# Optimization experiments

Measured on AMD Instinct MI355X. Metric: run time of the kernel, lower is better.

Reference implementation:

```python
import jax, jax.numpy as jnp
import numpy as np

N_NODES = 50000
N_EDGES = 800000
N_GRAPHS = 256
IN_DIM = 128
HID = 128
BN_EPS = 1e-5


def setup_inputs() -> dict:
    key = jax.random.key(0)
    ks = jax.random.split(key, 12)
    s = 1.0 / np.sqrt(HID)
    feats = jax.random.normal(ks[0], (N_NODES, IN_DIM), jnp.float32)
    src = jax.random.randint(ks[1], (2, N_EDGES), 0, N_NODES)
    dst = jax.random.randint(ks[2], (2, N_EDGES), 0, N_NODES)
    graph_ids = jnp.sort(jax.random.randint(ks[3], (N_NODES,), 0, N_GRAPHS))
    eps = jnp.full((2, 2), 0.1, jnp.float32)
    Wa = jax.random.normal(ks[4], (2, 2, IN_DIM, HID), jnp.float32) * s
    ba = jnp.zeros((2, 2, HID), jnp.float32)
    bng = jnp.ones((2, 2, HID), jnp.float32)
    bnb = jnp.zeros((2, 2, HID), jnp.float32)
    Wb = jax.random.normal(ks[5], (2, 2, HID, HID), jnp.float32) * s
    bb = jnp.zeros((2, 2, HID), jnp.float32)
    oW1 = jax.random.normal(ks[6], (2 * HID, HID), jnp.float32) * (1.0 / np.sqrt(2 * HID))
    ob1 = jnp.zeros((HID,), jnp.float32)
    oW2 = jax.random.normal(ks[7], (HID, HID), jnp.float32) * s
    ob2 = jnp.zeros((HID,), jnp.float32)
    oW3 = jax.random.normal(ks[8], (HID, 1), jnp.float32) * s
    ob3 = jnp.zeros((1,), jnp.float32)
    return {"feats": feats, "src": src, "dst": dst, "graph_ids": graph_ids,
            "n_graphs": N_GRAPHS, "eps": eps, "Wa": Wa, "ba": ba, "bng": bng,
            "bnb": bnb, "Wb": Wb, "bb": bb, "oW1": oW1, "ob1": ob1,
            "oW2": oW2, "ob2": ob2, "oW3": oW3, "ob3": ob3}


def _gin_layer(h, s, d, eps_l, Wa_l, ba_l, g_l, be_l, Wb_l, bb_l, relu_out):
    # sum-aggregate messages from src to dst over edge list
    N = h.shape[0]
    agg = jax.ops.segment_sum(h[s], d, num_segments=N)  # [N, D]
    x = (1.0 + eps_l) * h + agg
    # MLP_Layer: Linear -> BatchNorm(training stats) -> ReLU -> Linear
    x = x @ Wa_l + ba_l
    mu = jnp.mean(x, axis=0)
    var = jnp.var(x, axis=0)
    x = (x - mu) * jax.lax.rsqrt(var + BN_EPS) * g_l + be_l
    x = jax.nn.relu(x)
    x = x @ Wb_l + bb_l
    return jax.nn.relu(x) if relu_out else x  # GINConv activation (gin1 only)


def reference(feats, src, dst, graph_ids, n_graphs, eps, Wa, ba, bng, bnb,
              Wb, bb, oW1, ob1, oW2, ob2, oW3, ob3):
    outs = []
    for e in range(2):  # one BTGINs encoder per bottom edge type
        h = feats
        for l in range(2):  # gin1 (ReLU) then gin2 (no activation)
            h = _gin_layer(h, src[e], dst[e], eps[e, l], Wa[e, l], ba[e, l],
                           bng[e, l], bnb[e, l], Wb[e, l], bb[e, l], relu_out=(l == 0))
        outs.append(h)
    h = jnp.concatenate(outs, axis=-1)  # [N, 2*HID]
    # readout_nodes op='sum': per-graph segment sum
    hg = jax.ops.segment_sum(h, graph_ids, num_segments=n_graphs)  # [G, 2*HID]
    # out_layers: 3-layer MLP, no BN
    x = jax.nn.relu(hg @ oW1 + ob1)
    x = jax.nn.relu(x @ oW2 + ob2)
    return x @ oW3 + ob3  # [G, 1]
```

## Files before the change

kernel.cpp:

```cpp
#include <hip/hip_runtime.h>

#define NT 50000
#define NE 800000
#define NG 256
#define DIM 128
#define GEMM_B ((NT + 127) / 128)

#define NB 128
#define BW 391
#define PB 196
#define PCH 4096
#define HCN (NB * PB)

typedef short s16x8 __attribute__((ext_vector_type(8)));
typedef float f32x16 __attribute__((ext_vector_type(16)));

__device__ __forceinline__ unsigned short f32_to_bf16(float f) {
    unsigned int u = __float_as_uint(f);
    u += 0x7FFFu + ((u >> 16) & 1u);
    return (unsigned short)(u >> 16);
}
__device__ __forceinline__ float bf16_to_f32(unsigned short h) {
    return __uint_as_float(((unsigned int)h) << 16);
}

__global__ __launch_bounds__(256) void tobf16_kernel(const float* __restrict__ in,
                                                     unsigned short* __restrict__ out) {
    int i = blockIdx.x * 256 + threadIdx.x;
    if (i >= NT * 32) return;
    float4 v = ((const float4*)in)[i];
    ushort4 o;
    o.x = f32_to_bf16(v.x); o.y = f32_to_bf16(v.y);
    o.z = f32_to_bf16(v.z); o.w = f32_to_bf16(v.w);
    ((ushort4*)out)[i] = o;
}

__global__ __launch_bounds__(256) void csr_part_hist_kernel(
        const int* __restrict__ dstAll, int* __restrict__ hcoarseAll) {
    const int* dst = dstAll + (size_t)blockIdx.y * NE;
    int* hcoarse = hcoarseAll + (size_t)blockIdx.y * HCN;
    __shared__ int h[NB];
    if (threadIdx.x < NB) h[threadIdx.x] = 0;
    __syncthreads();
#pragma unroll
    for (int i = 0; i < PCH / 256; ++i) {
        int e = blockIdx.x * PCH + i * 256 + threadIdx.x;
        if (e < NE) atomicAdd(&h[dst[e] / BW], 1);
    }
    __syncthreads();
    if (threadIdx.x < NB)
        hcoarse[threadIdx.x * PB + blockIdx.x] = h[threadIdx.x];
}

__global__ __launch_bounds__(1024) void csr_scan_kernel(
        const int* __restrict__ hcoarseAll, int* __restrict__ offAll,
        int* __restrict__ bucketBaseAll, int* __restrict__ indptrAll) {
    const int* hcoarse = hcoarseAll + (size_t)blockIdx.x * HCN;
    int* off = offAll + (size_t)blockIdx.x * HCN;
    int* bucketBase = bucketBaseAll + (size_t)blockIdx.x * (NB + 1);
    int* indptr = indptrAll + (size_t)blockIdx.x * (NT + 1);
    __shared__ int ps[1024];
    int t = threadIdx.x;
    const int CH = (HCN + 1023) / 1024;
    int beg = t * CH, end = beg + CH; if (end > HCN) end = HCN;
    int s = 0;
    for (int i = beg; i < end; ++i) s += hcoarse[i];
    ps[t] = s;
    __syncthreads();
    for (int o = 1; o < 1024; o <<= 1) {
        int v = (t >= o) ? ps[t - o] : 0;
        __syncthreads();
        ps[t] += v;
        __syncthreads();
    }
    int run = (t == 0) ? 0 : ps[t - 1];
    for (int i = beg; i < end; ++i) {
        off[i] = run;
        if (i % PB == 0) bucketBase[i / PB] = run;
        run += hcoarse[i];
    }
    if (t == 1023) bucketBase[NB] = NE;
    if (t == 0) indptr[NT] = NE;
}

__global__ __launch_bounds__(256) void csr_scatter_kernel(
        const int* __restrict__ srcAll, const int* __restrict__ dstAll,
        const int* __restrict__ offAll, unsigned int* __restrict__ partAll) {
    const int* src = srcAll + (size_t)blockIdx.y * NE;
    const int* dst = dstAll + (size_t)blockIdx.y * NE;
    const int* off = offAll + (size_t)blockIdx.y * HCN;
    unsigned int* part = partAll + (size_t)blockIdx.y * NE;
    __shared__ int cur[NB];
    if (threadIdx.x < NB) cur[threadIdx.x] = off[threadIdx.x * PB + blockIdx.x];
    __syncthreads();
#pragma unroll
    for (int i = 0; i < PCH / 256; ++i) {
        int e = blockIdx.x * PCH + i * 256 + threadIdx.x;
        if (e < NE) {
            int d = dst[e];
            int b = d / BW;
            int pos = atomicAdd(&cur[b], 1);
            part[pos] = ((unsigned int)(d - b * BW) << 16) | (unsigned int)src[e];
        }
    }
}

__global__ __launch_bounds__(256) void csr_finalize_kernel(
        const unsigned int* __restrict__ partAll,
        const int* __restrict__ bucketBaseAll,
        int* __restrict__ indptrAll, int* __restrict__ esrcAll) {
    const unsigned int* part = partAll + (size_t)blockIdx.y * NE;
    const int* bucketBase = bucketBaseAll + (size_t)blockIdx.y * (NB + 1);
    int* indptr = indptrAll + (size_t)blockIdx.y * (NT + 1);
    int* esrc = esrcAll + (size_t)blockIdx.y * NE;
    __shared__ int cnt[512];
    __shared__ int excl[512];
    __shared__ int ps[256];
    __shared__ int cur[BW + 1];
    int b = blockIdx.x, t = threadIdx.x;
    int base = bucketBase[b];
    int n = bucketBase[b + 1] - base;
    cnt[t] = 0; cnt[t + 256] = 0;
    for (int j = t; j <= BW; j += 256) cur[j] = 0;
    __syncthreads();
    for (int i = t; i < n; i += 256) atomicAdd(&cnt[part[base + i] >> 16], 1);
    __syncthreads();
    int a0 = cnt[2 * t], a1 = cnt[2 * t + 1];
    ps[t] = a0 + a1;
    __syncthreads();
    for (int o = 1; o < 256; o <<= 1) {
        int v = (t >= o) ? ps[t - o] : 0;
        __syncthreads();
        ps[t] += v;
        __syncthreads();
    }
    int before = (t == 0) ? 0 : ps[t - 1];
    excl[2 * t] = before;
    excl[2 * t + 1] = before + a0;
    __syncthreads();
    int node0 = b * BW;
    for (int j = t; j < BW; j += 256) {
        int gn = node0 + j;
        if (gn < NT) indptr[gn] = base + excl[j];
    }
    for (int i = t; i < n; i += 256) {
        unsigned int pk = part[base + i];
        int dl = pk >> 16;
        int pos = atomicAdd(&cur[dl], 1);
        esrc[base + excl[dl] + pos] = (int)(pk & 0xFFFFu);
    }
}

__global__ __launch_bounds__(256) void agg_split_kernel(
        const float* __restrict__ h, long hStride,
        const unsigned short* __restrict__ hb, long hbStride,
        const int* __restrict__ indptr2, const int* __restrict__ esrc2,
        const float* __restrict__ eps_p, int l,
        unsigned short* __restrict__ xout2) {
    int e = blockIdx.y;
    const float* hs = h + (size_t)e * hStride;
    const unsigned short* hbs = hb + (size_t)e * hbStride;
    const int* indptr = indptr2 + (size_t)e * (NT + 1);
    const int* esrc = esrc2 + (size_t)e * NE;
    unsigned short* xo = xout2 + (size_t)e * NT * 256;
    int node = blockIdx.x * 4 + (threadIdx.x >> 6);
    if (node >= NT) return;
    int lane = threadIdx.x & 63;
    int half = lane >> 5, c = lane & 31;
    float s0 = 0.f, s1 = 0.f, s2 = 0.f, s3 = 0.f;
    if (half == 0) {
        float e1 = 1.0f + eps_p[e * 2 + l];
        float4 a = ((const float4*)hs)[(size_t)node * 32 + c];
        s0 = e1 * a.x; s1 = e1 * a.y; s2 = e1 * a.z; s3 = e1 * a.w;
    }
    int beg = indptr[node], end = indptr[node + 1];
    int deg = end - beg;
    int endFull = beg + (deg & ~15);
    int j = beg;
    for (; j < endFull; j += 16) {
        int b0 = j + half * 8;
        int idx[8];
#pragma unroll
        for (int k = 0; k < 8; ++k) idx[k] = esrc[b0 + k];
        ushort4 v[8];
#pragma unroll
        for (int k = 0; k < 8; ++k)
            v[k] = *(const ushort4*)(hbs + (size_t)idx[k] * 128 + c * 4);
#pragma unroll
        for (int k = 0; k < 8; ++k) {
            s0 += bf16_to_f32(v[k].x);
            s1 += bf16_to_f32(v[k].y);
            s2 += bf16_to_f32(v[k].z);
            s3 += bf16_to_f32(v[k].w);
        }
    }
    if (j < end) {
        int b0 = j + half * 8;
        int idx[8];
        float m[8];
#pragma unroll
        for (int k = 0; k < 8; ++k) {
            int jj = b0 + k;
            int ok = jj < end;
            idx[k] = esrc[ok ? jj : end - 1];
            m[k] = ok ? 1.f : 0.f;
        }
        ushort4 v[8];
#pragma unroll
        for (int k = 0; k < 8; ++k)
            v[k] = *(const ushort4*)(hbs + (size_t)idx[k] * 128 + c * 4);
#pragma unroll
        for (int k = 0; k < 8; ++k) {
            s0 = fmaf(bf16_to_f32(v[k].x), m[k], s0);
            s1 = fmaf(bf16_to_f32(v[k].y), m[k], s1);
            s2 = fmaf(bf16_to_f32(v[k].z), m[k], s2);
            s3 = fmaf(bf16_to_f32(v[k].w), m[k], s3);
        }
    }
    s0 += __shfl_xor(s0, 32);
    s1 += __shfl_xor(s1, 32);
    s2 += __shfl_xor(s2, 32);
    s3 += __shfl_xor(s3, 32);
    if (half == 0) {
        ushort4 hv, lv;
        hv.x = f32_to_bf16(s0); lv.x = f32_to_bf16(s0 - bf16_to_f32(hv.x));
        hv.y = f32_to_bf16(s1); lv.y = f32_to_bf16(s1 - bf16_to_f32(hv.y));
        hv.z = f32_to_bf16(s2); lv.z = f32_to_bf16(s2 - bf16_to_f32(hv.z));
        hv.w = f32_to_bf16(s3); lv.w = f32_to_bf16(s3 - bf16_to_f32(hv.w));
        *(ushort4*)(xo + (size_t)node * 256 + c * 4) = hv;
        *(ushort4*)(xo + (size_t)node * 256 + 128 + c * 4) = lv;
    }
}

__global__ __launch_bounds__(256) void bsplit_kernel(const float* __restrict__ Wa,
                                                     const float* __restrict__ Wb,
                                                     unsigned short* __restrict__ Bfrag,
                                                     const int* __restrict__ gid,
                                                     int* __restrict__ goff,
                                                     float* __restrict__ gsumAll) {
    if (blockIdx.x == 0) {
        int g = threadIdx.x;
        int lo = 0, hi = NT;
        while (lo < hi) {
            int mid = (lo + hi) >> 1;
            if (gid[mid] < g) lo = mid + 1; else hi = mid;
        }
        goff[g] = lo;
        if (g == 0) goff[NG] = NT;
    }
    if (blockIdx.x == 1) {
#pragma unroll
        for (int i = 0; i < 4; ++i) gsumAll[i * 256 + threadIdx.x] = 0.f;
    }
    int slot = blockIdx.x >> 3;
    int sub = blockIdx.x & 7;
    const float* W = (slot < 4) ? (Wa + (size_t)slot * DIM * DIM)
                                : (Wb + (size_t)(slot - 4) * DIM * DIM);
    unsigned short* out = Bfrag + (size_t)slot * 32768;
    for (int i = 0; i < 16; ++i) {
        int e = sub * 4096 + i * 256 + threadIdx.x;
        int kphys = e >> 7, n = e & 127;
        int k = kphys & 127;
        float wv = W[k * 128 + n];
        unsigned short hi = f32_to_bf16(wv);
        unsigned short val = (kphys < 128) ? hi : f32_to_bf16(wv - bf16_to_f32(hi));
        int nt = n >> 5, nin = n & 31;
        int kcp = kphys >> 4, kgp = (kphys >> 3) & 1, jj = kphys & 7;
        out[(size_t)(((nt * 16 + kcp) * 64) + kgp * 32 + nin) * 8 + jj] = val;
    }
}

template <int ASPLIT, int STATS, int RELU, int EMITB>
__global__ __launch_bounds__(256) void fused_gemm_kernel(
        const void* __restrict__ Asrc, long aStride,
        const unsigned short* __restrict__ BfragBase, int bOff, int l,
        const float* __restrict__ biasBase,
        const float* __restrict__ gsumBase,
        const float* __restrict__ gammaBase, const float* __restrict__ betaBase,
        float* __restrict__ C, long cStride,
        unsigned short* __restrict__ CBout, long cbStride,
        float* __restrict__ gsumOutBase) {
    __shared__ char smem[65536 + 1024];
    unsigned short* sB = (unsigned short*)smem;
    float* sBNa = (float*)(smem + 65536);
    float* sBNb = sBNa + 128;
    const int ety = blockIdx.y, wi = ety * 2 + l;
    const unsigned short* Bfrag = BfragBase + (size_t)(bOff + wi) * 32768;
    const float* bias = biasBase + (size_t)wi * DIM;
    const int tid = threadIdx.x;
    const int w = tid >> 6, lane = tid & 63;
    const int nin = lane & 31, kg = lane >> 5;
    const int row0 = blockIdx.x * 128;
    const int myrow = row0 + w * 32 + nin;
    const int rowc = myrow < NT ? myrow : NT - 1;

    {
        const uint4* Bg = (const uint4*)Bfrag;
        uint4* sB4 = (uint4*)smem;
#pragma unroll
        for (int i = 0; i < 16; ++i) sB4[tid + 256 * i] = Bg[tid + 256 * i];
    }

    s16x8 ahi[8], alo[8];
    if (ASPLIT) {
        const unsigned short* ar = (const unsigned short*)Asrc
                + (size_t)ety * aStride + (size_t)rowc * 256 + kg * 8;
#pragma unroll
        for (int kc = 0; kc < 8; ++kc) {
            ahi[kc] = *(const s16x8*)(ar + kc * 16);
            alo[kc] = *(const s16x8*)(ar + 128 + kc * 16);
        }
        __syncthreads();
    } else {
        const float* gsumIn = gsumBase + (size_t)wi * 256;
        if (tid < 128) {
            float mu = gsumIn[tid] * (1.0f / NT);
            float var = gsumIn[128 + tid] * (1.0f / NT) - mu * mu;
            float inv = rsqrtf(var + 1e-5f);
            float a = gammaBase[wi * DIM + tid] * inv;
            sBNa[tid] = a;
            sBNb[tid] = betaBase[wi * DIM + tid] - mu * a;
        }
        __syncthreads();
        const float* yr = (const float*)Asrc + (size_t)ety * aStride
                + (size_t)rowc * 128 + kg * 8;
#pragma unroll
        for (int kc = 0; kc < 8; ++kc) {
            int c0 = kc * 16 + kg * 8;
            float4 y0 = *(const float4*)(yr + kc * 16);
            float4 y1 = *(const float4*)(yr + kc * 16 + 4);
            float4 a0 = *(const float4*)(sBNa + c0);
            float4 a1 = *(const float4*)(sBNa + c0 + 4);
            float4 b0 = *(const float4*)(sBNb + c0);
            float4 b1 = *(const float4*)(sBNb + c0 + 4);
            float t[8];
            t[0] = fmaxf(0.f, fmaf(y0.x, a0.x, b0.x));
            t[1] = fmaxf(0.f, fmaf(y0.y, a0.y, b0.y));
            t[2] = fmaxf(0.f, fmaf(y0.z, a0.z, b0.z));
            t[3] = fmaxf(0.f, fmaf(y0.w, a0.w, b0.w));
            t[4] = fmaxf(0.f, fmaf(y1.x, a1.x, b1.x));
            t[5] = fmaxf(0.f, fmaf(y1.y, a1.y, b1.y));
            t[6] = fmaxf(0.f, fmaf(y1.z, a1.z, b1.z));
            t[7] = fmaxf(0.f, fmaf(y1.w, a1.w, b1.w));
            union { s16x8 v; unsigned short u[8]; } H, L;
#pragma unroll
            for (int q = 0; q < 8; ++q) {
                H.u[q] = f32_to_bf16(t[q]);
                L.u[q] = f32_to_bf16(t[q] - bf16_to_f32(H.u[q]));
            }
            ahi[kc] = H.v; alo[kc] = L.v;
        }
    }

    f32x16 acc[4];
#pragma unroll
    for (int nt = 0; nt < 4; ++nt)
#pragma unroll
        for (int r = 0; r < 16; ++r) acc[nt][r] = 0.f;

#pragma unroll
    for (int nt = 0; nt < 4; ++nt) {
        const unsigned short* bp = sB + (size_t)(nt * 16) * 512 + lane * 8;
#pragma unroll
        for (int kc = 0; kc < 8; ++kc) {
            s16x8 b = *(const s16x8*)(bp + kc * 512);
            acc[nt] = __builtin_amdgcn_mfma_f32_32x32x16_bf16(ahi[kc], b, acc[nt], 0, 0, 0);
            acc[nt] = __builtin_amdgcn_mfma_f32_32x32x16_bf16(alo[kc], b, acc[nt], 0, 0, 0);
        }
#pragma unroll
        for (int kc = 0; kc < 8; ++kc) {
            s16x8 b = *(const s16x8*)(bp + (8 + kc) * 512);
            acc[nt] = __builtin_amdgcn_mfma_f32_32x32x16_bf16(ahi[kc], b, acc[nt], 0, 0, 0);
        }
    }

    float* Ce = C + (size_t)ety * cStride;
    unsigned short* CBe = EMITB ? (CBout + (size_t)ety * cbStride) : nullptr;
    const int rbase = row0 + w * 32 + 4 * kg;
#pragma unroll
    for (int nt = 0; nt < 4; ++nt) {
        int col = nt * 32 + nin;
        float bv = bias[col];
#pragma unroll
        for (int reg = 0; reg < 16; ++reg) {
            int gr = rbase + (reg & 3) + 8 * (reg >> 2);
            float v = acc[nt][reg] + bv;
            if (RELU) v = fmaxf(v, 0.f);
            if (gr < NT) {
                Ce[(size_t)gr * 128 + col] = v;
                if (EMITB) CBe[(size_t)gr * 128 + col] = f32_to_bf16(v);
            }
            acc[nt][reg] = (gr < NT) ? v : 0.f;
        }
    }

    if (STATS) {
        float* gsum = gsumOutBase + (size_t)wi * 256;
        __syncthreads();
        float* ls = (float*)smem;
        ls[tid] = 0.f;
        __syncthreads();
#pragma unroll
        for (int nt = 0; nt < 4; ++nt) {
            int col = nt * 32 + nin;
            float s = 0.f, q = 0.f;
#pragma unroll
            for (int reg = 0; reg < 16; ++reg) { float v = acc[nt][reg]; s += v; q += v * v; }
            atomicAdd(&ls[col], s);
            atomicAdd(&ls[128 + col], q);
        }
        __syncthreads();
        if (tid < 128) {
            atomicAdd(&gsum[tid], ls[tid]);
            atomicAdd(&gsum[128 + tid], ls[128 + tid]);
        }
    }
}

__global__ __launch_bounds__(256) void readout_kernel(const float* __restrict__ bufH2,
                                                      const int* __restrict__ goff,
                                                      float* __restrict__ hgp) {
    int e = blockIdx.y;
    const float* h = bufH2 + (size_t)e * NT * 128;
    int colOff = e * 128;
    int g = blockIdx.x >> 1, h2 = blockIdx.x & 1;
    int c = threadIdx.x & 127, rr = threadIdx.x >> 7;
    int beg = goff[g], end = goff[g + 1];
    int n = beg + h2 * 2 + rr;
    float a0 = 0.f, a1 = 0.f, a2 = 0.f, a3 = 0.f;
    for (; n + 12 < end; n += 16) {
        a0 += h[(size_t)n * 128 + c];
        a1 += h[(size_t)(n + 4) * 128 + c];
        a2 += h[(size_t)(n + 8) * 128 + c];
        a3 += h[(size_t)(n + 12) * 128 + c];
    }
    for (; n < end; n += 4) a0 += h[(size_t)n * 128 + c];
    float acc = (a0 + a1) + (a2 + a3);
    __shared__ float ls[256];
    ls[threadIdx.x] = acc;
    __syncthreads();
    if (threadIdx.x < 128)
        hgp[(size_t)h2 * NG * 256 + g * 256 + colOff + c] = ls[c] + ls[128 + c];
}

__global__ __launch_bounds__(128) void mlp_kernel(const float* __restrict__ hgp,
                                                  const float* __restrict__ oW1,
                                                  const float* __restrict__ ob1,
                                                  const float* __restrict__ oW2,
                                                  const float* __restrict__ ob2,
                                                  const float* __restrict__ oW3,
                                                  const float* __restrict__ ob3,
                                                  float* __restrict__ out) {
    int g = blockIdx.x, t = threadIdx.x;
    __shared__ float sh[256];
    __shared__ float z[128];
    sh[t] = hgp[g * 256 + t] + hgp[(size_t)NG * 256 + g * 256 + t];
    sh[t + 128] = hgp[g * 256 + 128 + t] + hgp[(size_t)NG * 256 + g * 256 + 128 + t];
    __syncthreads();
    float acc = ob1[t];
    for (int k = 0; k < 256; ++k) acc = fmaf(sh[k], oW1[k * 128 + t], acc);
    float z1 = fmaxf(acc, 0.f);
    z[t] = z1;
    __syncthreads();
    acc = ob2[t];
    for (int k = 0; k < 128; ++k) acc = fmaf(z[k], oW2[k * 128 + t], acc);
    float z2 = fmaxf(acc, 0.f);
    float p = z2 * oW3[t];
    for (int off = 32; off > 0; off >>= 1) p += __shfl_down(p, off, 64);
    __shared__ float wsum[2];
    if ((t & 63) == 0) wsum[t >> 6] = p;
    __syncthreads();
    if (t == 0) out[g] = wsum[0] + wsum[1] + ob3[0];
}

extern "C" void kernel_launch(void* const* d_in, const int* in_sizes, int n_in,
                              void* d_out, int out_size, void* d_ws, size_t ws_size,
                              hipStream_t stream) {
    (void)in_sizes; (void)n_in; (void)out_size; (void)ws_size;
    const float* feats = (const float*)d_in[0];
    const int*   src   = (const int*)d_in[1];
    const int*   dst   = (const int*)d_in[2];
    const int*   gid   = (const int*)d_in[3];
    const float* epsp  = (const float*)d_in[5];
    const float* Wa    = (const float*)d_in[6];
    const float* ba    = (const float*)d_in[7];
    const float* bng   = (const float*)d_in[8];
    const float* bnb   = (const float*)d_in[9];
    const float* Wb    = (const float*)d_in[10];
    const float* bb    = (const float*)d_in[11];
    const float* oW1   = (const float*)d_in[12];
    const float* ob1   = (const float*)d_in[13];
    const float* oW2   = (const float*)d_in[14];
    const float* ob2   = (const float*)d_in[15];
    const float* oW3   = (const float*)d_in[16];
    const float* ob3   = (const float*)d_in[17];
    float* out = (float*)d_out;

    char* p = (char*)d_ws;
    auto carve = [&](size_t bytes) -> void* {
        void* r = (void*)p;
        p += (bytes + 255) & ~(size_t)255;
        return r;
    };
    unsigned short* Asplit2 = (unsigned short*)carve((size_t)2 * NT * 256 * 2);
    float* bufY2   = (float*)carve((size_t)2 * NT * DIM * 4);
    float* bufH2   = (float*)carve((size_t)2 * NT * DIM * 4);
    unsigned short* featsB = (unsigned short*)carve((size_t)NT * DIM * 2);
    unsigned short* hB2    = (unsigned short*)carve((size_t)2 * NT * DIM * 2);
    unsigned short* Bfrag  = (unsigned short*)carve((size_t)8 * 32768 * 2);
    int*   esrc2    = (int*)carve((size_t)2 * NE * 4);
    unsigned int* part2 = (unsigned int*)carve((size_t)2 * NE * 4);
    int*   hcoarse2 = (int*)carve((size_t)2 * HCN * 4);
    int*   offbuf2  = (int*)carve((size_t)2 * HCN * 4);
    int*   bb2      = (int*)carve((size_t)2 * (NB + 1) * 4);
    int*   indptr2  = (int*)carve((size_t)2 * (NT + 1) * 4);
    int*   goff     = (int*)carve((size_t)(NG + 1) * 4);
    float* gsumAll  = (float*)carve((size_t)4 * 256 * 4);
    float* hgp      = (float*)carve((size_t)2 * NG * 256 * 4);

    const int CB = (NT * 32 + 255) / 256;

    bsplit_kernel<<<64, 256, 0, stream>>>(Wa, Wb, Bfrag, gid, goff, gsumAll);
    tobf16_kernel<<<CB, 256, 0, stream>>>(feats, featsB);

    csr_part_hist_kernel<<<dim3(PB, 2), 256, 0, stream>>>(dst, hcoarse2);
    csr_scan_kernel<<<2, 1024, 0, stream>>>(hcoarse2, offbuf2, bb2, indptr2);
    csr_scatter_kernel<<<dim3(PB, 2), 256, 0, stream>>>(src, dst, offbuf2, part2);
    csr_finalize_kernel<<<dim3(NB, 2), 256, 0, stream>>>(part2, bb2, indptr2, esrc2);

    for (int l = 0; l < 2; ++l) {
        if (l == 0)
            agg_split_kernel<<<dim3((NT + 3) / 4, 2), 256, 0, stream>>>(
                feats, 0, featsB, 0, indptr2, esrc2, epsp, l, Asplit2);
        else
            agg_split_kernel<<<dim3((NT + 3) / 4, 2), 256, 0, stream>>>(
                bufH2, (long)NT * DIM, hB2, (long)NT * DIM,
                indptr2, esrc2, epsp, l, Asplit2);
        fused_gemm_kernel<1, 1, 0, 0><<<dim3(GEMM_B, 2), 256, 0, stream>>>(
            Asplit2, (long)NT * 256, Bfrag, 0, l, ba,
            nullptr, nullptr, nullptr,
            bufY2, (long)NT * DIM, nullptr, 0, gsumAll);
        if (l == 0)
            fused_gemm_kernel<0, 0, 1, 1><<<dim3(GEMM_B, 2), 256, 0, stream>>>(
                bufY2, (long)NT * DIM, Bfrag, 4, l, bb,
                gsumAll, bng, bnb,
                bufH2, (long)NT * DIM, hB2, (long)NT * DIM, nullptr);
        else
            fused_gemm_kernel<0, 0, 0, 0><<<dim3(GEMM_B, 2), 256, 0, stream>>>(
                bufY2, (long)NT * DIM, Bfrag, 4, l, bb,
                gsumAll, bng, bnb,
                bufH2, (long)NT * DIM, nullptr, 0, nullptr);
    }
    readout_kernel<<<dim3(NG * 2, 2), 256, 0, stream>>>(bufH2, goff, hgp);
    mlp_kernel<<<NG, 128, 0, stream>>>(hgp, oW1, ob1, oW2, ob2, oW3, ob3, out);
}
```

Baseline: 534.7 us.

## Fuse graph readout segment-sum into final GEMM epilogue via atomics

The last layer's second GEMM no longer writes its 50000x128 fp32 output per edge type. Its epilogue instead does run-length reduction over sorted graph ids per lane and atomically adds partial sums into a single per-graph buffer, which is zeroed by a memset. This removes the separate readout kernel and a large global write plus read. In exchange it adds float atomics, which make summation order nondeterministic, plus an extra memset launch.

After: 514.0 us. -3.9%, faster.

```diff
diff --git a/kernel.cpp b/kernel.cpp
--- a/kernel.cpp
+++ b/kernel.cpp
@@ -270,7 +270,7 @@
     }
 }
 
-template <int ASPLIT, int STATS, int RELU, int EMITB>
+template <int ASPLIT, int STATS, int RELU, int EMITB, int FUSERO>
 __global__ __launch_bounds__(256) void fused_gemm_kernel(
         const void* __restrict__ Asrc, long aStride,
         const unsigned short* __restrict__ BfragBase, int bOff, int l,
@@ -279,11 +279,13 @@
         const float* __restrict__ gammaBase, const float* __restrict__ betaBase,
         float* __restrict__ C, long cStride,
         unsigned short* __restrict__ CBout, long cbStride,
-        float* __restrict__ gsumOutBase) {
-    __shared__ char smem[65536 + 1024];
+        float* __restrict__ gsumOutBase,
+        const int* __restrict__ gidIn, float* __restrict__ hgpOut) {
+    __shared__ char smem[65536 + 1024 + 512];
     unsigned short* sB = (unsigned short*)smem;
     float* sBNa = (float*)(smem + 65536);
     float* sBNb = sBNa + 128;
+    int* sgid = (int*)(smem + 65536 + 1024);
     const int ety = blockIdx.y, wi = ety * 2 + l;
     const unsigned short* Bfrag = BfragBase + (size_t)(bOff + wi) * 32768;
     const float* bias = biasBase + (size_t)wi * DIM;
@@ -320,6 +322,10 @@
             float a = gammaBase[wi * DIM + tid] * inv;
             sBNa[tid] = a;
             sBNb[tid] = betaBase[wi * DIM + tid] - mu * a;
+            if (FUSERO) {
+                int rr = row0 + tid;
+                sgid[tid] = gidIn[rr < NT ? rr : NT - 1];
+            }
         }
         __syncthreads();
         const float* yr = (const float*)Asrc + (size_t)ety * aStride
@@ -374,6 +380,33 @@
         }
     }
 
+    if (FUSERO) {
+#pragma unroll
+        for (int nt = 0; nt < 4; ++nt) {
+            int col = nt * 32 + nin;
+            float bv = bias[col];
+            float run = 0.f;
+            int curg = -1;
+#pragma unroll
+            for (int reg = 0; reg < 16; ++reg) {
+                int lr = w * 32 + 4 * kg + (reg & 3) + 8 * (reg >> 2);
+                int gr = row0 + lr;
+                float v = acc[nt][reg] + bv;
+                int g = sgid[lr];
+                if (g != curg) {
+                    if (curg >= 0)
+                        atomicAdd(&hgpOut[(size_t)curg * 256 + ety * 128 + col], run);
+                    curg = g;
+                    run = 0.f;
+                }
+                run += (gr < NT) ? v : 0.f;
+            }
+            if (curg >= 0)
+                atomicAdd(&hgpOut[(size_t)curg * 256 + ety * 128 + col], run);
+        }
+        return;
+    }
+
     float* Ce = C + (size_t)ety * cStride;
     unsigned short* CBe = EMITB ? (CBout + (size_t)ety * cbStride) : nullptr;
     const int rbase = row0 + w * 32 + 4 * kg;
@@ -415,32 +448,6 @@
             atomicAdd(&gsum[128 + tid], ls[128 + tid]);
         }
     }
-}
-
-__global__ __launch_bounds__(256) void readout_kernel(const float* __restrict__ bufH2,
-                                                      const int* __restrict__ goff,
-                                                      float* __restrict__ hgp) {
-    int e = blockIdx.y;
-    const float* h = bufH2 + (size_t)e * NT * 128;
-    int colOff = e * 128;
-    int g = blockIdx.x >> 1, h2 = blockIdx.x & 1;
-    int c = threadIdx.x & 127, rr = threadIdx.x >> 7;
-    int beg = goff[g], end = goff[g + 1];
-    int n = beg + h2 * 2 + rr;
-    float a0 = 0.f, a1 = 0.f, a2 = 0.f, a3 = 0.f;
-    for (; n + 12 < end; n += 16) {
-        a0 += h[(size_t)n * 128 + c];
-        a1 += h[(size_t)(n + 4) * 128 + c];
-        a2 += h[(size_t)(n + 8) * 128 + c];
-        a3 += h[(size_t)(n + 12) * 128 + c];
-    }
-    for (; n < end; n += 4) a0 += h[(size_t)n * 128 + c];
-    float acc = (a0 + a1) + (a2 + a3);
-    __shared__ float ls[256];
-    ls[threadIdx.x] = acc;
-    __syncthreads();
-    if (threadIdx.x < 128)
-        hgp[(size_t)h2 * NG * 256 + g * 256 + colOff + c] = ls[c] + ls[128 + c];
 }
 
 __global__ __launch_bounds__(128) void mlp_kernel(const float* __restrict__ hgp,
@@ -454,8 +461,8 @@
     int g = blockIdx.x, t = threadIdx.x;
     __shared__ float sh[256];
     __shared__ float z[128];
-    sh[t] = hgp[g * 256 + t] + hgp[(size_t)NG * 256 + g * 256 + t];
-    sh[t + 128] = hgp[g * 256 + 128 + t] + hgp[(size_t)NG * 256 + g * 256 + 128 + t];
+    sh[t] = hgp[g * 256 + t];
+    sh[t + 128] = hgp[g * 256 + 128 + t];
     __syncthreads();
     float acc = ob1[t];
     for (int k = 0; k < 256; ++k) acc = fmaf(sh[k], oW1[k * 128 + t], acc);
@@ -516,12 +523,13 @@
     int*   indptr2  = (int*)carve((size_t)2 * (NT + 1) * 4);
     int*   goff     = (int*)carve((size_t)(NG + 1) * 4);
     float* gsumAll  = (float*)carve((size_t)4 * 256 * 4);
-    float* hgp      = (float*)carve((size_t)2 * NG * 256 * 4);
+    float* hgp      = (float*)carve((size_t)NG * 256 * 4);
 
     const int CB = (NT * 32 + 255) / 256;
 
     bsplit_kernel<<<64, 256, 0, stream>>>(Wa, Wb, Bfrag, gid, goff, gsumAll);
     tobf16_kernel<<<CB, 256, 0, stream>>>(feats, featsB);
+    hipMemsetAsync(hgp, 0, (size_t)NG * 256 * 4, stream);
 
     csr_part_hist_kernel<<<dim3(PB, 2), 256, 0, stream>>>(dst, hcoarse2);
     csr_scan_kernel<<<2, 1024, 0, stream>>>(hcoarse2, offbuf2, bb2, indptr2);
@@ -536,21 +544,23 @@
             agg_split_kernel<<<dim3((NT + 3) / 4, 2), 256, 0, stream>>>(
                 bufH2, (long)NT * DIM, hB2, (long)NT * DIM,
                 indptr2, esrc2, epsp, l, Asplit2);
-        fused_gemm_kernel<1, 1, 0, 0><<<dim3(GEMM_B, 2), 256, 0, stream>>>(
+        fused_gemm_kernel<1, 1, 0, 0, 0><<<dim3(GEMM_B, 2), 256, 0, stream>>>(
             Asplit2, (long)NT * 256, Bfrag, 0, l, ba,
             nullptr, nullptr, nullptr,
-            bufY2, (long)NT * DIM, nullptr, 0, gsumAll);
+            bufY2, (long)NT * DIM, nullptr, 0, gsumAll,
+            nullptr, nullptr);
         if (l == 0)
-            fused_gemm_kernel<0, 0, 1, 1><<<dim3(GEMM_B, 2), 256, 0, stream>>>(
+            fused_gemm_kernel<0, 0, 1, 1, 0><<<dim3(GEMM_B, 2), 256, 0, stream>>>(
                 bufY2, (long)NT * DIM, Bfrag, 4, l, bb,
                 gsumAll, bng, bnb,
-                bufH2, (long)NT * DIM, hB2, (long)NT * DIM, nullptr);
+                bufH2, (long)NT * DIM, hB2, (long)NT * DIM, nullptr,
+                nullptr, nullptr);
         else
-            fused_gemm_kernel<0, 0, 0, 0><<<dim3(GEMM_B, 2), 256, 0, stream>>>(
+            fused_gemm_kernel<0, 0, 0, 0, 1><<<dim3(GEMM_B, 2), 256, 0, stream>>>(
                 bufY2, (long)NT * DIM, Bfrag, 4, l, bb,
                 gsumAll, bng, bnb,
-                bufH2, (long)NT * DIM, nullptr, 0, nullptr);
-    }
-    readout_kernel<<<dim3(NG * 2, 2), 256, 0, stream>>>(bufH2, goff, hgp);
+                nullptr, 0, nullptr, 0, nullptr,
+                gid, hgp);
+    }
     mlp_kernel<<<NG, 128, 0, stream>>>(hgp, oW1, ob1, oW2, ob2, oW3, ob3, out);
 }
```
